# Performance work log

Measured on AMD Instinct MI355X. Metric: run time of the kernel, lower is better.

Reference implementation:

```python
import jax, jax.numpy as jnp
import numpy as np

N_EMBD = 1024
N_HEADS = 16
D_K = N_EMBD // N_HEADS


def setup_inputs() -> dict:
    key = jax.random.key(0)
    k1, k2, k3, k4, k5 = jax.random.split(key, 5)
    B, T, E = 4, 2048, N_EMBD
    scale = 1.0 / np.sqrt(E)
    inputs = jax.random.normal(k1, (B, T, E), dtype=jnp.float32)
    W_qkv = jax.random.normal(k2, (3 * E, E), dtype=jnp.float32) * scale
    b_qkv = jax.random.normal(k3, (3 * E,), dtype=jnp.float32) * 0.01
    W_out = jax.random.normal(k4, (E, E), dtype=jnp.float32) * scale
    b_out = jax.random.normal(k5, (E,), dtype=jnp.float32) * 0.01
    return {"inputs": inputs, "W_qkv": W_qkv, "b_qkv": b_qkv,
            "W_out": W_out, "b_out": b_out}


def reference(inputs, W_qkv, b_qkv, W_out, b_out):
    B, T, E = inputs.shape
    H, dk = N_HEADS, D_K
    # fused QKV projection: [B,T,3E]
    qkv = jnp.einsum('bte,fe->btf', inputs, W_qkv) + b_qkv
    # reshape to [B,T,H,3*dk] then to [B,H,T,3*dk], split into q,k,v
    qkv = qkv.reshape(B, T, H, 3 * dk).transpose(0, 2, 1, 3)
    q, k, v = jnp.split(qkv, 3, axis=-1)  # each [B,H,T,dk]
    scores = jnp.einsum('bhqd,bhkd->bhqk', q, k) / np.sqrt(dk)
    causal = jnp.tril(jnp.ones((T, T), dtype=bool))
    scores = jnp.where(causal, scores, -jnp.inf)
    attn = jax.nn.softmax(scores, axis=-1)
    out = jnp.einsum('bhqk,bhkd->bhqd', attn, v)  # [B,H,T,dk]
    out = out.transpose(0, 2, 1, 3).reshape(B, T, E)
    return jnp.einsum('bte,fe->btf', out, W_out) + b_out
```

## Files before the change

### kernel.cpp

```cpp
#include <hip/hip_runtime.h>
#include <stdint.h>


#define DEVFN static __device__ __forceinline__

typedef __attribute__((ext_vector_type(8))) __bf16 bf16x8;
typedef __attribute__((ext_vector_type(8))) ushort ushort8v;
typedef __attribute__((ext_vector_type(4))) float float4v;

#define AS1 __attribute__((address_space(1)))
#define AS3 __attribute__((address_space(3)))

DEVFN ushort f2bf(float f) {
  __bf16 h = (__bf16)f;
  union { __bf16 h; ushort u; } c; c.h = h;
  return c.u;
}

__global__ void cast3_f32_bf16(const float* __restrict__ a, int na,
                               const float* __restrict__ b, int nb,
                               const float* __restrict__ c, int nc,
                               ushort* __restrict__ out) {
  int total = na + nb + nc;
  int stride = gridDim.x * blockDim.x * 4;
  for (int j = (blockIdx.x * blockDim.x + threadIdx.x) * 4; j + 3 < total; j += stride) {
    const float* src;
    if (j < na) src = a + j;
    else if (j < na + nb) src = b + (j - na);
    else src = c + (j - na - nb);
    float4 v = *reinterpret_cast<const float4*>(src);
    ushort4 o;
    o.x = f2bf(v.x); o.y = f2bf(v.y); o.z = f2bf(v.z); o.w = f2bf(v.w);
    *reinterpret_cast<ushort4*>(out + j) = o;
  }
}

template<bool OUT_BF16, bool QSCALE, bool V_SPLIT>
__global__ __launch_bounds__(256) void gemm_bt(
    const ushort* __restrict__ A, const ushort* __restrict__ B,
    const float* __restrict__ bias, void* __restrict__ Cout,
    ushort* __restrict__ vt,
    int M, int N, int K) {
  __shared__ ushort lds_a[2][128 * 32];
  __shared__ ushort lds_b[2][128 * 32];
  const int tid = threadIdx.x;
  const int lane = tid & 63;
  const int w = tid >> 6;
  const int wr = w >> 1, wc = w & 1;
  const int l15 = lane & 15, lg = lane >> 4;

  const int nwg = (int)(gridDim.x * gridDim.y);
  const int orig = (int)(blockIdx.y * gridDim.x + blockIdx.x);
  const int cpx = nwg >> 3;
  const int swz = ((orig & 7) * cpx) + (orig >> 3);
  const int bx = swz % (int)gridDim.x, by = swz / (int)gridDim.x;
  const int m0 = by * 128, n0 = bx * 128;

  const int srow = tid >> 2;
  const int sch = tid & 3;
  const int schs = sch ^ ((srow >> 1) & 3);
  const ushort* ga0 = A + (size_t)(m0 + srow) * K + schs * 8;
  const ushort* gb0 = B + (size_t)(n0 + srow) * K + schs * 8;
  const ushort* ga1 = A + (size_t)(m0 + srow + 64) * K + schs * 8;
  const ushort* gb1 = B + (size_t)(n0 + srow + 64) * K + schs * 8;

#define STAGE(buf, k0)                                                                             \
  {                                                                                                \
    __builtin_amdgcn_global_load_lds((const AS1 uint32_t*)(ga0 + (k0)), (AS3 uint32_t*)&lds_a[buf][tid * 8], 16, 0, 0);        \
    __builtin_amdgcn_global_load_lds((const AS1 uint32_t*)(gb0 + (k0)), (AS3 uint32_t*)&lds_b[buf][tid * 8], 16, 0, 0);        \
    __builtin_amdgcn_global_load_lds((const AS1 uint32_t*)(ga1 + (k0)), (AS3 uint32_t*)&lds_a[buf][2048 + tid * 8], 16, 0, 0); \
    __builtin_amdgcn_global_load_lds((const AS1 uint32_t*)(gb1 + (k0)), (AS3 uint32_t*)&lds_b[buf][2048 + tid * 8], 16, 0, 0); \
  }

  float4v acc[4][4] = {};

  STAGE(0, 0);
  __syncthreads();

  int cur = 0;
  for (int k0 = 0; k0 < K; k0 += 32) {
    if (k0 + 32 < K) STAGE(cur ^ 1, k0 + 32);

    bf16x8 af[4], bfr[4];
#pragma unroll
    for (int m = 0; m < 4; ++m) {
      int row = wr * 64 + m * 16 + l15;
      af[m] = *reinterpret_cast<const bf16x8*>(&lds_a[cur][row * 32 + ((lg ^ ((row >> 1) & 3)) * 8)]);
    }
#pragma unroll
    for (int n = 0; n < 4; ++n) {
      int row = wc * 64 + n * 16 + l15;
      bfr[n] = *reinterpret_cast<const bf16x8*>(&lds_b[cur][row * 32 + ((lg ^ ((row >> 1) & 3)) * 8)]);
    }
    __builtin_amdgcn_s_setprio(1);
#pragma unroll
    for (int m = 0; m < 4; ++m)
#pragma unroll
      for (int n = 0; n < 4; ++n)
        acc[m][n] = __builtin_amdgcn_mfma_f32_16x16x32_bf16(af[m], bfr[n], acc[m][n], 0, 0, 0);
    __builtin_amdgcn_s_setprio(0);

    __syncthreads();
    cur ^= 1;
  }
#undef STAGE

#pragma unroll
  for (int n = 0; n < 4; ++n) {
    int col = n0 + wc * 64 + n * 16 + l15;
    float bv = bias[col];
    int seg = (col % 192) >> 6;
    float f = (QSCALE && seg == 0) ? 0.125f * 1.44269504f : 1.0f;
    if (V_SPLIT && seg == 2) {
      int h = col / 192;
      int d = (col % 192) - 128;
#pragma unroll
      for (int m = 0; m < 4; ++m) {
#pragma unroll
        for (int r = 0; r < 4; ++r) {
          int rowg = m0 + wr * 64 + m * 16 + lg * 4 + r;
          int bb = rowg >> 11, tt = rowg & 2047;
          vt[((size_t)(bb * 16 + h) * 64 + d) * 2048 + tt] = f2bf(acc[m][n][r] + bv);
        }
      }
    } else {
#pragma unroll
      for (int m = 0; m < 4; ++m) {
#pragma unroll
        for (int r = 0; r < 4; ++r) {
          int rowg = m0 + wr * 64 + m * 16 + lg * 4 + r;
          float vv = (acc[m][n][r] + bv) * f;
          if (OUT_BF16)
            ((ushort*)Cout)[(size_t)rowg * N + col] = f2bf(vv);
          else
            ((float*)Cout)[(size_t)rowg * N + col] = vv;
        }
      }
    }
  }
}

__global__ __launch_bounds__(256) void transpose_v(
    const ushort* __restrict__ qkv, ushort* __restrict__ vt) {
  const int bh = blockIdx.y, b = bh >> 4, h = bh & 15;
  const int w = threadIdx.x >> 6, lane = threadIdx.x & 63;
  const int tc = lane >> 3, dc = lane & 7;
  const int t0 = blockIdx.x * 256 + w * 64 + tc * 8;

  const ushort* src = qkv + (size_t)(b * 2048 + t0) * 3072 + h * 192 + 128 + dc * 8;
  ushort r[8][8];
#pragma unroll
  for (int i = 0; i < 8; ++i) {
    ushort8v v = *reinterpret_cast<const ushort8v*>(src + (size_t)i * 3072);
#pragma unroll
    for (int j = 0; j < 8; ++j) r[i][j] = v[j];
  }
  ushort* dst = vt + ((size_t)bh * 64 + dc * 8) * 2048 + t0;
#pragma unroll
  for (int j = 0; j < 8; ++j) {
    ushort8v o;
#pragma unroll
    for (int i = 0; i < 8; ++i) o[i] = r[i][j];
    *reinterpret_cast<ushort8v*>(dst + (size_t)j * 2048) = o;
  }
}

__global__ __launch_bounds__(512, 6) void attn_kernel(
    const ushort* __restrict__ qkv, const ushort* __restrict__ vt,
    ushort* __restrict__ out) {
  __shared__ ushort k_lds[2][4096];
  __shared__ ushort v_lds[2][4096];
  __shared__ ushort p_lds[8][1024];

  const int qb = (int)gridDim.y - 1 - (int)blockIdx.y;
  const int bh = blockIdx.x;
  const int b = bh >> 4, h = bh & 15;
  const int tid = threadIdx.x, lane = tid & 63, w = tid >> 6;
  const int l15 = lane & 15, lg = lane >> 4;

  const size_t rs = 3072;
  const ushort* qbase = qkv + (size_t)(b * 2048) * rs + h * 192;
  const ushort* kbase = qbase + 64;
  const ushort* vtbase = vt + (size_t)bh * 64 * 2048;

  const int q0 = qb * 128;
  const int q0w = q0 + w * 16;
  const int nt = (qb + 1) * 2;

  bf16x8 qf[2];
#pragma unroll
  for (int kk = 0; kk < 2; ++kk)
    qf[kk] = *reinterpret_cast<const bf16x8*>(
        qbase + (size_t)(q0w + l15) * rs + kk * 32 + lg * 8);

  bf16x8 ones;
#pragma unroll
  for (int e = 0; e < 8; ++e) ones[e] = (__bf16)1.0f;

  const int srow = w * 8 + (lane >> 3);
  const int sch = (lane & 7) ^ ((lane >> 3) & 7);
  const ushort* ksrc = kbase + (size_t)srow * rs + sch * 8;
  const ushort* vsrc = vtbase + (size_t)srow * 2048 + sch * 8;
  const size_t kstep = (size_t)64 * rs;
  const size_t vstep = 64;

  __builtin_amdgcn_global_load_lds((const AS1 uint32_t*)ksrc, (AS3 uint32_t*)&k_lds[0][w * 512 + lane * 8], 16, 0, 0);
  __builtin_amdgcn_global_load_lds((const AS1 uint32_t*)vsrc, (AS3 uint32_t*)&v_lds[0][w * 512 + lane * 8], 16, 0, 0);
  ksrc += kstep; vsrc += vstep;
  __syncthreads();

  float4v oacc[4] = {};
  float4v lacc = {};

  int cur = 0;
  for (int t = 0; t < nt; ++t) {
    if (t + 1 < nt) {
      __builtin_amdgcn_global_load_lds((const AS1 uint32_t*)ksrc, (AS3 uint32_t*)&k_lds[cur ^ 1][w * 512 + lane * 8], 16, 0, 0);
      __builtin_amdgcn_global_load_lds((const AS1 uint32_t*)vsrc, (AS3 uint32_t*)&v_lds[cur ^ 1][w * 512 + lane * 8], 16, 0, 0);
      ksrc += kstep; vsrc += vstep;
    }

    if (t * 64 <= q0w + 15) {
      const ushort* kb = k_lds[cur];
      float4v s[4] = {};
      __builtin_amdgcn_s_setprio(1);
#pragma unroll
      for (int kk = 0; kk < 2; ++kk)
#pragma unroll
        for (int n = 0; n < 4; ++n) {
          int row = n * 16 + l15;
          bf16x8 kf = *reinterpret_cast<const bf16x8*>(&kb[row * 64 + (((kk * 4 + lg) ^ (row & 7)) * 8)]);
          s[n] = __builtin_amdgcn_mfma_f32_16x16x32_bf16(qf[kk], kf, s[n], 0, 0, 0);
        }
      __builtin_amdgcn_s_setprio(0);

      if (t * 64 + 63 > q0w) {
#pragma unroll
        for (int n = 0; n < 4; ++n) {
          int kvg = t * 64 + n * 16 + l15;
#pragma unroll
          for (int r = 0; r < 4; ++r) {
            int qg = q0w + lg * 4 + r;
            if (kvg > qg) s[n][r] = -1e30f;
          }
        }
      }

#pragma unroll
      for (int n = 0; n < 4; ++n) {
#pragma unroll
        for (int r = 0; r < 4; ++r) {
          float p = __builtin_amdgcn_exp2f(s[n][r]);
          int row = lg * 4 + r;
          int col = n * 16 + l15;
          int ch = (col >> 3) ^ (row & 7);
          p_lds[w][row * 64 + ch * 8 + (col & 7)] = f2bf(p);
        }
      }

      bf16x8 pf[2];
#pragma unroll
      for (int kk = 0; kk < 2; ++kk)
        pf[kk] = *reinterpret_cast<const bf16x8*>(&p_lds[w][l15 * 64 + (((kk * 4 + lg) ^ (l15 & 7)) * 8)]);

      const ushort* vb_ = v_lds[cur];
      __builtin_amdgcn_s_setprio(1);
#pragma unroll
      for (int kk = 0; kk < 2; ++kk) {
#pragma unroll
        for (int nd = 0; nd < 4; ++nd) {
          int vr = nd * 16 + l15;
          bf16x8 vf = *reinterpret_cast<const bf16x8*>(&vb_[vr * 64 + (((kk * 4 + lg) ^ (vr & 7)) * 8)]);
          oacc[nd] = __builtin_amdgcn_mfma_f32_16x16x32_bf16(pf[kk], vf, oacc[nd], 0, 0, 0);
        }
        lacc = __builtin_amdgcn_mfma_f32_16x16x32_bf16(pf[kk], ones, lacc, 0, 0, 0);
      }
      __builtin_amdgcn_s_setprio(0);
    }

    __syncthreads();
    cur ^= 1;
  }

#pragma unroll
  for (int nd = 0; nd < 4; ++nd) {
#pragma unroll
    for (int r = 0; r < 4; ++r) {
      int qg = q0 + w * 16 + lg * 4 + r;
      int col = h * 64 + nd * 16 + l15;
      out[(size_t)(b * 2048 + qg) * 1024 + col] = f2bf(oacc[nd][r] / lacc[r]);
    }
  }
}

extern "C" void kernel_launch(void* const* d_in, const int* in_sizes, int n_in,
                              void* d_out, int out_size, void* d_ws, size_t ws_size,
                              hipStream_t stream) {
  (void)in_sizes; (void)n_in; (void)out_size;
  const float* x      = (const float*)d_in[0];
  const float* w_qkv  = (const float*)d_in[1];
  const float* b_qkv  = (const float*)d_in[2];
  const float* w_out  = (const float*)d_in[3];
  const float* b_out  = (const float*)d_in[4];
  float* outp = (float*)d_out;

  const int BT = 4 * 2048;
  const int E = 1024, N3 = 3072;

  char* ws = (char*)d_ws;
  ushort* xb    = (ushort*)ws;  ws += (size_t)BT * E * 2;
  ushort* wqkvb = (ushort*)ws;  ws += (size_t)N3 * E * 2;
  ushort* woutb = (ushort*)ws;  ws += (size_t)E * E * 2;
  ushort* qkvb  = (ushort*)ws;  ws += (size_t)BT * N3 * 2;
  ushort* attb  = (ushort*)ws;  ws += (size_t)BT * E * 2;
  ushort* vtsep = (ushort*)ws;  ws += (size_t)BT * E * 2;
  const size_t needed = (size_t)(ws - (char*)d_ws);
  const bool vsplit = (ws_size >= needed);

  cast3_f32_bf16<<<2048, 256, 0, stream>>>(x, BT * E, w_qkv, N3 * E, w_out, E * E, xb);

  dim3 g1(N3 / 128, BT / 128);
  dim3 gt(8, 64);
  dim3 g2(64, 16);
  dim3 g3(E / 128, BT / 128);

  if (vsplit) {
    gemm_bt<true, true, true><<<g1, 256, 0, stream>>>(xb, wqkvb, b_qkv, qkvb, vtsep, BT, N3, E);
    attn_kernel<<<g2, 512, 0, stream>>>(qkvb, vtsep, attb);
  } else {
    ushort* vtb = xb;
    gemm_bt<true, true, false><<<g1, 256, 0, stream>>>(xb, wqkvb, b_qkv, qkvb, nullptr, BT, N3, E);
    transpose_v<<<gt, 256, 0, stream>>>(qkvb, vtb);
    attn_kernel<<<g2, 512, 0, stream>>>(qkvb, vtb, attb);
  }

  gemm_bt<false, false, false><<<g3, 256, 0, stream>>>(attb, woutb, b_out, outp, nullptr, BT, E, E);
}
```

Before: 171.7 us.

## Compute transposed scores and pass P to PV MFMA via lane shuffles instead of LDS

Swaps the QK^T MFMA operands so each lane holds scores for one query row across several keys. This lets the bf16-packed probabilities be redistributed into the A-operand layout with cross-lane shuffles, removing the per-wave P scratch buffer in LDS and its store/load round trip. The row sum is now accumulated in registers and reduced with shuffles at the end, replacing the extra ones-vector MFMA, and division becomes a reciprocal multiply. In exchange it adds shuffle instructions and selects, and the approximate reciprocal may change rounding slightly. LDS use also drops, which may allow more occupancy.

```diff
diff --git a/kernel.cpp b/kernel.cpp
--- a/kernel.cpp
+++ b/kernel.cpp
@@ -15,6 +15,9 @@
   __bf16 h = (__bf16)f;
   union { __bf16 h; ushort u; } c; c.h = h;
   return c.u;
+}
+DEVFN uint32_t pack2bf(float lo, float hi) {
+  return ((uint32_t)f2bf(hi) << 16) | (uint32_t)f2bf(lo);
 }
 
 __global__ void cast3_f32_bf16(const float* __restrict__ a, int na,
@@ -170,7 +173,6 @@
     ushort* __restrict__ out) {
   __shared__ ushort k_lds[2][4096];
   __shared__ ushort v_lds[2][4096];
-  __shared__ ushort p_lds[8][1024];
 
   const int qb = (int)gridDim.y - 1 - (int)blockIdx.y;
   const int bh = blockIdx.x;
@@ -193,9 +195,9 @@
     qf[kk] = *reinterpret_cast<const bf16x8*>(
         qbase + (size_t)(q0w + l15) * rs + kk * 32 + lg * 8);
 
-  bf16x8 ones;
-#pragma unroll
-  for (int e = 0; e < 8; ++e) ones[e] = (__bf16)1.0f;
+  const int la = l15 + 32 * (lg & 1);
+  const int lb = la + 16;
+  const bool sel = ((lg >> 1) & 1) != 0;
 
   const int srow = w * 8 + (lane >> 3);
   const int sch = (lane & 7) ^ ((lane >> 3) & 7);
@@ -210,7 +212,7 @@
   __syncthreads();
 
   float4v oacc[4] = {};
-  float4v lacc = {};
+  float lsum = 0.f;
 
   int cur = 0;
   for (int t = 0; t < nt; ++t) {
@@ -230,65 +232,79 @@
         for (int n = 0; n < 4; ++n) {
           int row = n * 16 + l15;
           bf16x8 kf = *reinterpret_cast<const bf16x8*>(&kb[row * 64 + (((kk * 4 + lg) ^ (row & 7)) * 8)]);
-          s[n] = __builtin_amdgcn_mfma_f32_16x16x32_bf16(qf[kk], kf, s[n], 0, 0, 0);
+          s[n] = __builtin_amdgcn_mfma_f32_16x16x32_bf16(kf, qf[kk], s[n], 0, 0, 0);
         }
       __builtin_amdgcn_s_setprio(0);
 
       if (t * 64 + 63 > q0w) {
+        int qg = q0w + l15;
 #pragma unroll
         for (int n = 0; n < 4; ++n) {
-          int kvg = t * 64 + n * 16 + l15;
 #pragma unroll
           for (int r = 0; r < 4; ++r) {
-            int qg = q0w + lg * 4 + r;
+            int kvg = t * 64 + n * 16 + lg * 4 + r;
             if (kvg > qg) s[n][r] = -1e30f;
           }
         }
       }
 
-#pragma unroll
-      for (int n = 0; n < 4; ++n) {
+      float ls = 0.f;
+#pragma unroll
+      for (int n = 0; n < 4; ++n)
 #pragma unroll
         for (int r = 0; r < 4; ++r) {
           float p = __builtin_amdgcn_exp2f(s[n][r]);
-          int row = lg * 4 + r;
-          int col = n * 16 + l15;
-          int ch = (col >> 3) ^ (row & 7);
-          p_lds[w][row * 64 + ch * 8 + (col & 7)] = f2bf(p);
-        }
-      }
-
-      bf16x8 pf[2];
-#pragma unroll
-      for (int kk = 0; kk < 2; ++kk)
-        pf[kk] = *reinterpret_cast<const bf16x8*>(&p_lds[w][l15 * 64 + (((kk * 4 + lg) ^ (l15 & 7)) * 8)]);
+          s[n][r] = p;
+          ls += p;
+        }
+      lsum += ls;
 
       const ushort* vb_ = v_lds[cur];
-      __builtin_amdgcn_s_setprio(1);
 #pragma unroll
       for (int kk = 0; kk < 2; ++kk) {
+        const int n0 = 2 * kk, n1 = n0 + 1;
+        uint32_t u00 = pack2bf(s[n0][0], s[n0][1]);
+        uint32_t u01 = pack2bf(s[n0][2], s[n0][3]);
+        uint32_t u10 = pack2bf(s[n1][0], s[n1][1]);
+        uint32_t u11 = pack2bf(s[n1][2], s[n1][3]);
+        int a00 = __shfl((int)u00, la); int a01 = __shfl((int)u01, la);
+        int a10 = __shfl((int)u10, la); int a11 = __shfl((int)u11, la);
+        int b00 = __shfl((int)u00, lb); int b01 = __shfl((int)u01, lb);
+        int b10 = __shfl((int)u10, lb); int b11 = __shfl((int)u11, lb);
+        union { uint32_t u[4]; bf16x8 v; } pf;
+        pf.u[0] = (uint32_t)(sel ? a10 : a00);
+        pf.u[1] = (uint32_t)(sel ? a11 : a01);
+        pf.u[2] = (uint32_t)(sel ? b10 : b00);
+        pf.u[3] = (uint32_t)(sel ? b11 : b01);
+
+        __builtin_amdgcn_s_setprio(1);
 #pragma unroll
         for (int nd = 0; nd < 4; ++nd) {
           int vr = nd * 16 + l15;
           bf16x8 vf = *reinterpret_cast<const bf16x8*>(&vb_[vr * 64 + (((kk * 4 + lg) ^ (vr & 7)) * 8)]);
-          oacc[nd] = __builtin_amdgcn_mfma_f32_16x16x32_bf16(pf[kk], vf, oacc[nd], 0, 0, 0);
-        }
-        lacc = __builtin_amdgcn_mfma_f32_16x16x32_bf16(pf[kk], ones, lacc, 0, 0, 0);
+          oacc[nd] = __builtin_amdgcn_mfma_f32_16x16x32_bf16(pf.v, vf, oacc[nd], 0, 0, 0);
+        }
+        __builtin_amdgcn_s_setprio(0);
       }
-      __builtin_amdgcn_s_setprio(0);
     }
 
     __syncthreads();
     cur ^= 1;
   }
 
+  lsum += __shfl_xor(lsum, 16);
+  lsum += __shfl_xor(lsum, 32);
+  float linv[4];
+#pragma unroll
+  for (int r = 0; r < 4; ++r)
+    linv[r] = __builtin_amdgcn_rcpf(__shfl(lsum, lg * 4 + r));
 #pragma unroll
   for (int nd = 0; nd < 4; ++nd) {
 #pragma unroll
     for (int r = 0; r < 4; ++r) {
       int qg = q0 + w * 16 + lg * 4 + r;
       int col = h * 64 + nd * 16 + l15;
-      out[(size_t)(b * 2048 + qg) * 1024 + col] = f2bf(oacc[nd][r] / lacc[r]);
+      out[(size_t)(b * 2048 + qg) * 1024 + col] = f2bf(oacc[nd][r] * linv[r]);
     }
   }
 }
```

Result: slower. 177.5 us (+3.4%).
